# Optimization experiments

Measured on AMD Instinct MI355X. Metric: run time of the kernel, lower is better.

## Reference

```python
import jax, jax.numpy as jnp
import numpy as np

N, E, H, C, NG = 50000, 800000, 4, 64, 32
HC = H * C  # 256


def setup_inputs() -> dict:
    key = jax.random.key(0)
    ks = jax.random.split(key, 32)
    f32 = jnp.float32
    def rn(k, shape, s=0.1):
        return jax.random.normal(k, shape, dtype=f32) * s
    inp = {}
    inp['x'] = jax.random.normal(ks[0], (N, 4), dtype=f32)
    inp['edge_index'] = jax.random.randint(ks[1], (2, E), 0, N, dtype=jnp.int32)
    inp['edge_attr'] = jax.random.normal(ks[2], (E, 1), dtype=f32)
    inp['batch'] = jnp.sort(jax.random.randint(ks[3], (N,), 0, NG, dtype=jnp.int32))
    # encoder
    inp['enc_w'] = rn(ks[4], (4, 64)); inp['enc_b'] = rn(ks[5], (64,))
    # GATv2 layer 1: in 64 -> H*C (lin_l source, lin_r target, lin_edge, att, bias)
    inp['g1_wl'] = rn(ks[6], (64, HC)); inp['g1_bl'] = rn(ks[7], (HC,))
    inp['g1_wr'] = rn(ks[8], (64, HC)); inp['g1_br'] = rn(ks[9], (HC,))
    inp['g1_we'] = rn(ks[10], (1, HC))
    inp['g1_att'] = rn(ks[11], (H, C))
    inp['g1_bias'] = rn(ks[12], (HC,))
    # GATv2 layer 2: in 256 -> H*C
    inp['g2_wl'] = rn(ks[13], (HC, HC)); inp['g2_bl'] = rn(ks[14], (HC,))
    inp['g2_wr'] = rn(ks[15], (HC, HC)); inp['g2_br'] = rn(ks[16], (HC,))
    inp['g2_we'] = rn(ks[17], (1, HC))
    inp['g2_att'] = rn(ks[18], (H, C))
    inp['g2_bias'] = rn(ks[19], (HC,))
    # post MLP: 256 -> 128 (LayerNorm, ReLU) -> 64 (ReLU)
    inp['p1_w'] = rn(ks[20], (HC, 128)); inp['p1_b'] = rn(ks[21], (128,))
    inp['ln_g'] = jnp.ones((128,), dtype=f32); inp['ln_b'] = jnp.zeros((128,), dtype=f32)
    inp['p2_w'] = rn(ks[22], (128, 64)); inp['p2_b'] = rn(ks[23], (64,))
    return inp


def _gatv2_layer(x, src, dst, eattr, wl, bl, wr, br, we, att, bias):
    # PyG GATv2Conv: alpha_e = att . leaky_relu(lin_l(x_src) + lin_r(x_dst) + lin_edge(e))
    n = x.shape[0]
    xl = (x @ wl + bl).reshape(n, H, C)   # source-side messages
    xr = (x @ wr + br).reshape(n, H, C)   # target-side
    e = (eattr @ we).reshape(-1, H, C)
    m = jax.nn.leaky_relu(xl[src] + xr[dst] + e, 0.2)        # [E',H,C]
    alpha = jnp.einsum('ehc,hc->eh', m, att)                  # [E',H]
    amax = jax.lax.stop_gradient(jax.ops.segment_max(alpha, dst, num_segments=n))
    ex = jnp.exp(alpha - amax[dst])
    den = jax.ops.segment_sum(ex, dst, num_segments=n)
    a = ex / den[dst]                                          # softmax per dst node
    out = jax.ops.segment_sum(a[:, :, None] * xl[src], dst, num_segments=n)
    return out.reshape(n, HC) + bias


def reference(x, edge_index, edge_attr, batch, enc_w, enc_b,
              g1_wl, g1_bl, g1_wr, g1_br, g1_we, g1_att, g1_bias,
              g2_wl, g2_bl, g2_wr, g2_br, g2_we, g2_att, g2_bias,
              p1_w, p1_b, ln_g, ln_b, p2_w, p2_b):
    n = x.shape[0]
    src0, dst0 = edge_index[0], edge_index[1]
    # PyG default add_self_loops=True with fill_value='mean' for edge_attr
    deg = jnp.maximum(jax.ops.segment_sum(jnp.ones_like(edge_attr[:, 0]), dst0, num_segments=n), 1.0)
    loop_attr = jax.ops.segment_sum(edge_attr, dst0, num_segments=n) / deg[:, None]
    idx = jnp.arange(n, dtype=src0.dtype)
    src = jnp.concatenate([src0, idx]); dst = jnp.concatenate([dst0, idx])
    eattr = jnp.concatenate([edge_attr, loop_attr], axis=0)
    h = jax.nn.relu(x @ enc_w + enc_b)
    h = jax.nn.relu(_gatv2_layer(h, src, dst, eattr, g1_wl, g1_bl, g1_wr, g1_br, g1_we, g1_att, g1_bias))
    h = jax.nn.relu(_gatv2_layer(h, src, dst, eattr, g2_wl, g2_bl, g2_wr, g2_br, g2_we, g2_att, g2_bias))
    # global mean pool over graphs
    cnt = jnp.maximum(jax.ops.segment_sum(jnp.ones((n,), h.dtype), batch, num_segments=NG), 1.0)
    g = jax.ops.segment_sum(h, batch, num_segments=NG) / cnt[:, None]
    # post MLP (dropout is identity in eval)
    z = g @ p1_w + p1_b
    mu = jnp.mean(z, axis=-1, keepdims=True)
    var = jnp.mean((z - mu) ** 2, axis=-1, keepdims=True)
    z = (z - mu) / jnp.sqrt(var + 1e-5) * ln_g + ln_b
    z = jax.nn.relu(z)
    z = jax.nn.relu(z @ p2_w + p2_b)
    return z
```

## Files before the change

kernel.cpp:

```cpp
#include <hip/hip_runtime.h>

#define CDIV(a,b) (((a)+(b)-1)/(b))

typedef __bf16 bf16_t;
typedef bf16_t bf16x8 __attribute__((ext_vector_type(8)));
typedef bf16_t bf16x4 __attribute__((ext_vector_type(4)));
typedef float floatx4 __attribute__((ext_vector_type(4)));
typedef float floatx2 __attribute__((ext_vector_type(2)));

__device__ __forceinline__ int sigma(int p) {
    return ((p >> 7) << 7) + ((p & 7) << 4) + ((p >> 3) & 15);
}

__global__ void k_deg(const int* __restrict__ ei, const float* __restrict__ ea,
                      float* __restrict__ deg, float* __restrict__ lsum, int E) {
    int e = blockIdx.x * 256 + threadIdx.x;
    if (e >= E) return;
    int d = ei[E + e];
    atomicAdd(&deg[d], 1.0f);
    atomicAdd(&lsum[d], ea[e]);
}

__global__ void k_loopattr(float* __restrict__ lsum, const float* __restrict__ deg, int n) {
    int i = blockIdx.x * 256 + threadIdx.x;
    if (i >= n) return;
    lsum[i] = lsum[i] / fmaxf(deg[i], 1.0f);
}

__global__ void k_scanA(const float* __restrict__ deg, int* __restrict__ part, int n) {
    __shared__ int sh[256];
    int t = threadIdx.x;
    int i = blockIdx.x * 256 + t;
    int v = (i < n) ? (int)deg[i] + 1 : 0;
    sh[t] = v;
    __syncthreads();
    for (int d = 128; d > 0; d >>= 1) { if (t < d) sh[t] += sh[t + d]; __syncthreads(); }
    if (t == 0) part[blockIdx.x] = sh[0];
}
__global__ void k_scanB(int* __restrict__ part, int nb) {
    __shared__ int sh[256];
    int t = threadIdx.x;
    int v = (t < nb) ? part[t] : 0;
    sh[t] = v;
    __syncthreads();
    for (int d = 1; d < 256; d <<= 1) {
        int u = (t >= d) ? sh[t - d] : 0;
        __syncthreads();
        sh[t] += u;
        __syncthreads();
    }
    if (t < nb) part[t] = sh[t] - v;
}
__global__ void k_scanC(const float* __restrict__ deg, const int* __restrict__ part,
                        int* __restrict__ off, int n) {
    __shared__ int sh[256];
    int t = threadIdx.x;
    int i = blockIdx.x * 256 + t;
    int v = (i < n) ? (int)deg[i] + 1 : 0;
    sh[t] = v;
    __syncthreads();
    for (int d = 1; d < 256; d <<= 1) {
        int u = (t >= d) ? sh[t - d] : 0;
        __syncthreads();
        sh[t] += u;
        __syncthreads();
    }
    int excl = part[blockIdx.x] + sh[t] - v;
    if (i < n) off[i] = excl;
    if (i == n - 1) off[n] = excl + v;
}

__global__ void k_fill(const int* __restrict__ ei, const float* __restrict__ ea,
                       const float* __restrict__ lattr, const int* __restrict__ off,
                       int* __restrict__ cursor, int* __restrict__ csr_src,
                       float* __restrict__ csr_ea, int E, int n) {
    int e = blockIdx.x * 256 + threadIdx.x;
    int EE = E + n;
    if (e >= EE) return;
    int s, d; float a;
    if (e < E) { s = ei[e]; d = ei[E + e]; a = ea[e]; }
    else       { s = e - E; d = s;         a = lattr[s]; }
    int pos = off[d] + atomicAdd(&cursor[d], 1);
    csr_src[pos] = s;
    csr_ea[pos] = a;
}

__global__ void k_enc(const float* __restrict__ x, const float* __restrict__ w,
                      const float* __restrict__ b, bf16_t* __restrict__ h0, int n) {
    int idx = blockIdx.x * 256 + threadIdx.x;
    if (idx >= n * 64) return;
    int nn = idx >> 6, j = idx & 63;
    const float* xr = x + (size_t)nn * 4;
    float s = b[j];
#pragma unroll
    for (int k = 0; k < 4; ++k) s = fmaf(xr[k], w[k * 64 + j], s);
    h0[idx] = (bf16_t)fmaxf(s, 0.0f);
}

__global__ void k_wcast2(const float* __restrict__ Wl, const float* __restrict__ Wr,
                         const float* __restrict__ bl, const float* __restrict__ br,
                         bf16_t* __restrict__ Wt, float* __restrict__ bias2,
                         int K, int kshift, int permK,
                         const float* __restrict__ we, const float* __restrict__ att,
                         const float* __restrict__ cb,
                         float* __restrict__ wep, float* __restrict__ attp,
                         float* __restrict__ cbp) {
    int idx = blockIdx.x * 256 + threadIdx.x;
    if (idx < 512) bias2[idx] = (idx < 256) ? bl[idx] : br[idx - 256];
    if (idx < 256) {
        int sg = sigma(idx);
        wep[idx] = we[sg]; attp[idx] = att[sg]; cbp[idx] = cb[sg];
    }
    if (idx >= 512 * K) return;
    int nn = idx >> kshift, k = idx & (K - 1);
    int ks = permK ? sigma(k) : k;
    float v = (nn < 256) ? Wl[ks * 256 + nn] : Wr[ks * 256 + (nn - 256)];
    Wt[idx] = (bf16_t)v;
}

__global__ __launch_bounds__(256) void k_gemm_mfma(
        const bf16_t* __restrict__ Hb, const bf16_t* __restrict__ Wt,
        const float* __restrict__ bias2, bf16_t* __restrict__ XL,
        bf16_t* __restrict__ XR, int nrows, int K) {
    __shared__ bf16_t As[128 * 32];
    __shared__ bf16_t Bs[128 * 32];
    int tid = threadIdx.x;
    int w = tid >> 6, lane = tid & 63;
    int quad = lane >> 4, m = lane & 15;
    int row0 = blockIdx.x * 128;
    int n0 = blockIdx.y * 128;
    floatx4 acc[2][8];
#pragma unroll
    for (int rt = 0; rt < 2; ++rt)
#pragma unroll
        for (int ct = 0; ct < 8; ++ct)
            acc[rt][ct] = (floatx4){0.f, 0.f, 0.f, 0.f};

    for (int k0 = 0; k0 < K; k0 += 32) {
        __syncthreads();
#pragma unroll
        for (int i = 0; i < 2; ++i) {
            int c = tid + i * 256;
            int r = c >> 2, kc = c & 3;
            int sw = (kc + (r >> 1)) & 3;
            int gr = row0 + r; if (gr >= nrows) gr = nrows - 1;
            bf16x8 v = *(const bf16x8*)&Hb[(size_t)gr * K + k0 + kc * 8];
            *(bf16x8*)&As[r * 32 + sw * 8] = v;
        }
#pragma unroll
        for (int i = 0; i < 2; ++i) {
            int c = tid + i * 256;
            int r = c >> 2, kc = c & 3;
            int sw = (kc + (r >> 1)) & 3;
            bf16x8 v = *(const bf16x8*)&Wt[(size_t)(n0 + r) * K + k0 + kc * 8];
            *(bf16x8*)&Bs[r * 32 + sw * 8] = v;
        }
        __syncthreads();
        bf16x8 af[2], bfr[8];
#pragma unroll
        for (int rt = 0; rt < 2; ++rt) {
            int ar = w * 32 + rt * 16 + m;
            af[rt] = *(bf16x8*)&As[ar * 32 + (((quad + (ar >> 1)) & 3) * 8)];
        }
#pragma unroll
        for (int ct = 0; ct < 8; ++ct) {
            int br = ct * 16 + m;
            bfr[ct] = *(bf16x8*)&Bs[br * 32 + (((quad + (br >> 1)) & 3) * 8)];
        }
#pragma unroll
        for (int ct = 0; ct < 8; ++ct) {
            acc[0][ct] = __builtin_amdgcn_mfma_f32_16x16x32_bf16(af[0], bfr[ct], acc[0][ct], 0, 0, 0);
            acc[1][ct] = __builtin_amdgcn_mfma_f32_16x16x32_bf16(af[1], bfr[ct], acc[1][ct], 0, 0, 0);
        }
    }
    int tile = (n0 >> 7) & 1;
    bf16_t* dst = (n0 < 256) ? XL : XR;
    float bv[8];
#pragma unroll
    for (int ct = 0; ct < 8; ++ct) bv[ct] = bias2[n0 + ct * 16 + m];
#pragma unroll
    for (int rt = 0; rt < 2; ++rt) {
#pragma unroll
        for (int i = 0; i < 4; ++i) {
            int row = row0 + w * 32 + rt * 16 + quad * 4 + i;
            if (row < nrows) {
                bf16x8 v;
#pragma unroll
                for (int ct = 0; ct < 8; ++ct) v[ct] = (bf16_t)(acc[rt][ct][i] + bv[ct]);
                *(bf16x8*)&dst[(size_t)row * 256 + tile * 128 + m * 8] = v;
            }
        }
    }
}

__device__ __forceinline__ void edge_step(
        int p, const int* __restrict__ csr_src, const float* __restrict__ csr_ea,
        const bf16_t* __restrict__ XL, int lane8,
        floatx2 xr01, floatx2 xr23, floatx2 wv01, floatx2 wv23,
        floatx2 av01, floatx2 av23,
        float& s, floatx2& a01, floatx2& a23) {
    int src = csr_src[p];
    float eav = csr_ea[p];
    uint2 u = *(const uint2*)((const char*)XL + (size_t)src * 512 + lane8);
    floatx2 x01, x23;
    x01.x = __uint_as_float(u.x << 16);
    x01.y = __uint_as_float(u.x & 0xffff0000u);
    x23.x = __uint_as_float(u.y << 16);
    x23.y = __uint_as_float(u.y & 0xffff0000u);
    floatx2 t01 = x01 + xr01 + eav * wv01;
    floatx2 t23 = x23 + xr23 + eav * wv23;
    t01 = __builtin_elementwise_max(t01, 0.2f * t01);
    t23 = __builtin_elementwise_max(t23, 0.2f * t23);
    floatx2 d = t01 * av01 + t23 * av23;
    float al = d.x + d.y;
    al += __shfl_xor(al, 2);
    al += __shfl_xor(al, 4);
    al += __shfl_xor(al, 8);
    al += __shfl_xor(al, 16);
    float wg = exp2f(al);
    s += wg;
    a01 += wg * x01;
    a23 += wg * x23;
}

__global__ void k_conv(const bf16_t* __restrict__ XL, const bf16_t* __restrict__ XR,
                       const float* __restrict__ wep, const float* __restrict__ attp,
                       const int* __restrict__ csr_src, const float* __restrict__ csr_ea,
                       const int* __restrict__ off, const float* __restrict__ cbp,
                       bf16_t* __restrict__ outb, int n) {
    int wid = (blockIdx.x * 256 + threadIdx.x) >> 6;
    int lane = threadIdx.x & 63;
    if (wid >= n) return;
    int lane8 = lane * 8;
    uint2 ur = *(const uint2*)((const char*)XR + (size_t)wid * 512 + lane8);
    floatx2 xr01, xr23;
    xr01.x = __uint_as_float(ur.x << 16);
    xr01.y = __uint_as_float(ur.x & 0xffff0000u);
    xr23.x = __uint_as_float(ur.y << 16);
    xr23.y = __uint_as_float(ur.y & 0xffff0000u);
    float4 wv = ((const float4*)wep)[lane];
    float4 av = ((const float4*)attp)[lane];
    floatx2 wv01 = {wv.x, wv.y}, wv23 = {wv.z, wv.w};
    floatx2 av01 = {av.x * 1.44269504f, av.y * 1.44269504f};
    floatx2 av23 = {av.z * 1.44269504f, av.w * 1.44269504f};
    int p0 = off[wid], p1 = off[wid + 1];
    float s = 0.f;
    floatx2 a01 = {0.f, 0.f}, a23 = {0.f, 0.f};
    int p = p0;
    for (; p + 1 < p1; p += 2) {
        edge_step(p,     csr_src, csr_ea, XL, lane8, xr01, xr23, wv01, wv23, av01, av23, s, a01, a23);
        edge_step(p + 1, csr_src, csr_ea, XL, lane8, xr01, xr23, wv01, wv23, av01, av23, s, a01, a23);
    }
    if (p < p1)
        edge_step(p,     csr_src, csr_ea, XL, lane8, xr01, xr23, wv01, wv23, av01, av23, s, a01, a23);
    float inv = 1.0f / s;
    float4 bv = ((const float4*)cbp)[lane];
    float o0 = fmaxf(fmaf(a01.x, inv, bv.x), 0.f);
    float o1 = fmaxf(fmaf(a01.y, inv, bv.y), 0.f);
    float o2 = fmaxf(fmaf(a23.x, inv, bv.z), 0.f);
    float o3 = fmaxf(fmaf(a23.y, inv, bv.w), 0.f);
    bf16x4 ob;
    ob.x = (bf16_t)o0; ob.y = (bf16_t)o1; ob.z = (bf16_t)o2; ob.w = (bf16_t)o3;
    *(bf16x4*)&outb[(size_t)wid * 256 + lane * 4] = ob;
}

__global__ void k_pool(const bf16_t* __restrict__ h, const int* __restrict__ batch,
                       float* __restrict__ gsum, float* __restrict__ gcnt, int n) {
    int j = threadIdx.x;
    int start = blockIdx.x * 64;
    if (start >= n) return;
    int end = start + 64; if (end > n) end = n;
    int cur = batch[start];
    float acc = 0.0f, cnt = 0.0f;
    for (int i = start; i < end; ++i) {
        int g = batch[i];
        if (g != cur) {
            atomicAdd(&gsum[cur * 256 + j], acc);
            if (j == 0) atomicAdd(&gcnt[cur], cnt);
            acc = 0.0f; cnt = 0.0f; cur = g;
        }
        acc += (float)h[(size_t)i * 256 + j];
        cnt += 1.0f;
    }
    atomicAdd(&gsum[cur * 256 + j], acc);
    if (j == 0) atomicAdd(&gcnt[cur], cnt);
}

__global__ void k_mlp(const float* __restrict__ gsum, const float* __restrict__ gcnt,
                      const float* __restrict__ p1w, const float* __restrict__ p1b,
                      const float* __restrict__ lng, const float* __restrict__ lnb,
                      const float* __restrict__ p2w, const float* __restrict__ p2b,
                      float* __restrict__ out) {
    int g = blockIdx.x;
    int t = threadIdx.x;
    __shared__ float gv[256];
    __shared__ float z[128];
    __shared__ float red[128];
    float invc = 1.0f / fmaxf(gcnt[g], 1.0f);
    gv[sigma(t)]       = gsum[g * 256 + t] * invc;
    gv[sigma(t + 128)] = gsum[g * 256 + 128 + t] * invc;
    __syncthreads();
    float z1 = p1b[t];
    for (int k = 0; k < 256; ++k) z1 = fmaf(gv[k], p1w[k * 128 + t], z1);
    red[t] = z1;
    __syncthreads();
    for (int d = 64; d > 0; d >>= 1) { if (t < d) red[t] += red[t + d]; __syncthreads(); }
    float mu = red[0] * (1.0f / 128.0f);
    __syncthreads();
    float dz = z1 - mu;
    red[t] = dz * dz;
    __syncthreads();
    for (int d = 64; d > 0; d >>= 1) { if (t < d) red[t] += red[t + d]; __syncthreads(); }
    float var = red[0] * (1.0f / 128.0f);
    float zn = dz * rsqrtf(var + 1e-5f) * lng[t] + lnb[t];
    z[t] = fmaxf(zn, 0.0f);
    __syncthreads();
    if (t < 64) {
        float o = p2b[t];
        for (int k = 0; k < 128; ++k) o = fmaf(z[k], p2w[k * 64 + t], o);
        out[g * 64 + t] = fmaxf(o, 0.0f);
    }
}

extern "C" void kernel_launch(void* const* d_in, const int* in_sizes, int n_in,
                              void* d_out, int out_size, void* d_ws, size_t ws_size,
                              hipStream_t stream) {
    const float* x      = (const float*)d_in[0];
    const int*   ei     = (const int*)d_in[1];
    const float* ea     = (const float*)d_in[2];
    const int*   batch  = (const int*)d_in[3];
    const float* enc_w  = (const float*)d_in[4];
    const float* enc_b  = (const float*)d_in[5];
    const float* g1_wl  = (const float*)d_in[6];
    const float* g1_bl  = (const float*)d_in[7];
    const float* g1_wr  = (const float*)d_in[8];
    const float* g1_br  = (const float*)d_in[9];
    const float* g1_we  = (const float*)d_in[10];
    const float* g1_att = (const float*)d_in[11];
    const float* g1_bias= (const float*)d_in[12];
    const float* g2_wl  = (const float*)d_in[13];
    const float* g2_bl  = (const float*)d_in[14];
    const float* g2_wr  = (const float*)d_in[15];
    const float* g2_br  = (const float*)d_in[16];
    const float* g2_we  = (const float*)d_in[17];
    const float* g2_att = (const float*)d_in[18];
    const float* g2_bias= (const float*)d_in[19];
    const float* p1_w   = (const float*)d_in[20];
    const float* p1_b   = (const float*)d_in[21];
    const float* ln_g   = (const float*)d_in[22];
    const float* ln_b   = (const float*)d_in[23];
    const float* p2_w   = (const float*)d_in[24];
    const float* p2_b   = (const float*)d_in[25];
    float* out = (float*)d_out;

    const int N  = in_sizes[3];
    const int E  = in_sizes[1] / 2;
    const int EE = E + N;
    const int NB = CDIV(N, 256);

    bf16_t* XL  = (bf16_t*)d_ws;
    bf16_t* XR  = XL + (size_t)N * 256;
    bf16_t* Hb  = XR + (size_t)N * 256;
    bf16_t* Wt  = Hb + (size_t)N * 256;
    float* csr_ea= (float*)(Wt + 512 * 256);
    float* bias2 = csr_ea + EE;
    float* wep   = bias2 + 512;
    float* attp  = wep + 256;
    float* cbp   = attp + 256;
    float* deg   = cbp + 256;
    float* lsum  = deg + N;
    float* gsum  = lsum + N;
    float* gcnt  = gsum + 32 * 256;
    int*   cursor= (int*)(gcnt + 32);
    int*   part  = cursor + N;
    int*   off   = part + 256;
    int*   csr_src = off + (N + 1);

    hipMemsetAsync(deg, 0, (size_t)(3 * N + 32 * 256 + 32) * sizeof(float), stream);

    k_deg<<<CDIV(E, 256), 256, 0, stream>>>(ei, ea, deg, lsum, E);
    k_loopattr<<<CDIV(N, 256), 256, 0, stream>>>(lsum, deg, N);
    k_scanA<<<NB, 256, 0, stream>>>(deg, part, N);
    k_scanB<<<1, 256, 0, stream>>>(part, NB);
    k_scanC<<<NB, 256, 0, stream>>>(deg, part, off, N);
    k_fill<<<CDIV(EE, 256), 256, 0, stream>>>(ei, ea, lsum, off, cursor, csr_src, csr_ea, E, N);
    k_enc<<<CDIV(N * 64, 256), 256, 0, stream>>>(x, enc_w, enc_b, Hb, N);

    dim3 ggrid(CDIV(N, 128), 4);

    k_wcast2<<<CDIV(512 * 64, 256), 256, 0, stream>>>(g1_wl, g1_wr, g1_bl, g1_br, Wt, bias2,
                                                      64, 6, 0, g1_we, g1_att, g1_bias,
                                                      wep, attp, cbp);
    k_gemm_mfma<<<ggrid, 256, 0, stream>>>(Hb, Wt, bias2, XL, XR, N, 64);
    k_conv<<<CDIV(N, 4), 256, 0, stream>>>(XL, XR, wep, attp, csr_src, csr_ea, off, cbp, Hb, N);

    k_wcast2<<<CDIV(512 * 256, 256), 256, 0, stream>>>(g2_wl, g2_wr, g2_bl, g2_br, Wt, bias2,
                                                       256, 8, 1, g2_we, g2_att, g2_bias,
                                                       wep, attp, cbp);
    k_gemm_mfma<<<ggrid, 256, 0, stream>>>(Hb, Wt, bias2, XL, XR, N, 256);
    k_conv<<<CDIV(N, 4), 256, 0, stream>>>(XL, XR, wep, attp, csr_src, csr_ea, off, cbp, Hb, N);

    k_pool<<<CDIV(N, 64), 256, 0, stream>>>(Hb, batch, gsum, gcnt, N);
    k_mlp<<<32, 128, 0, stream>>>(gsum, gcnt, p1_w, p1_b, ln_g, ln_b, p2_w, p2_b, out);
}
```

Measured before the change: 510.9 us.

## Split conv wavefront into two half-waves processing alternate edges with 16-byte gathers

The aggregation kernel now has each 32-lane half of a wavefront handle a different edge, each lane owning 8 channels loaded as one 16-byte gather. This halves the shuffle reduction depth per edge and doubles the edges in flight. The GEMM output layout and channel permutation (sigma2) change to match, and the half-wave partial sums are combined with a cross-half shuffle at the end. Pooling blocks also shrink to 32 rows for more parallelism. The cost is odd-degree padding work and extra final shuffles.

```diff
diff --git a/kernel.cpp b/kernel.cpp
--- a/kernel.cpp
+++ b/kernel.cpp
@@ -8,8 +8,16 @@
 typedef float floatx4 __attribute__((ext_vector_type(4)));
 typedef float floatx2 __attribute__((ext_vector_type(2)));
 
-__device__ __forceinline__ int sigma(int p) {
-    return ((p >> 7) << 7) + ((p & 7) << 4) + ((p >> 3) & 15);
+__device__ __forceinline__ int sigma2(int p) {
+    int tile = p >> 7, hh = (p >> 6) & 1, m = (p >> 2) & 15, c = p & 3;
+    return tile * 128 + (hh * 4 + c) * 16 + m;
+}
+
+__device__ __forceinline__ floatx2 up2(unsigned v) {
+    floatx2 r;
+    r.x = __uint_as_float(v << 16);
+    r.y = __uint_as_float(v & 0xffff0000u);
+    return r;
 }
 
 __global__ void k_deg(const int* __restrict__ ei, const float* __restrict__ ea,
@@ -108,12 +116,12 @@
     int idx = blockIdx.x * 256 + threadIdx.x;
     if (idx < 512) bias2[idx] = (idx < 256) ? bl[idx] : br[idx - 256];
     if (idx < 256) {
-        int sg = sigma(idx);
+        int sg = sigma2(idx);
         wep[idx] = we[sg]; attp[idx] = att[sg]; cbp[idx] = cb[sg];
     }
     if (idx >= 512 * K) return;
     int nn = idx >> kshift, k = idx & (K - 1);
-    int ks = permK ? sigma(k) : k;
+    int ks = permK ? sigma2(k) : k;
     float v = (nn < 256) ? Wl[ks * 256 + nn] : Wr[ks * 256 + (nn - 256)];
     Wt[idx] = (bf16_t)v;
 }
@@ -184,43 +192,50 @@
         for (int i = 0; i < 4; ++i) {
             int row = row0 + w * 32 + rt * 16 + quad * 4 + i;
             if (row < nrows) {
-                bf16x8 v;
-#pragma unroll
-                for (int ct = 0; ct < 8; ++ct) v[ct] = (bf16_t)(acc[rt][ct][i] + bv[ct]);
-                *(bf16x8*)&dst[(size_t)row * 256 + tile * 128 + m * 8] = v;
+                bf16x4 v0, v1;
+#pragma unroll
+                for (int ct = 0; ct < 4; ++ct) {
+                    v0[ct] = (bf16_t)(acc[rt][ct][i] + bv[ct]);
+                    v1[ct] = (bf16_t)(acc[rt][ct + 4][i] + bv[ct + 4]);
+                }
+                *(bf16x4*)&dst[(size_t)row * 256 + tile * 128 + m * 4] = v0;
+                *(bf16x4*)&dst[(size_t)row * 256 + tile * 128 + 64 + m * 4] = v1;
             }
         }
     }
 }
 
-__device__ __forceinline__ void edge_step(
-        int p, const int* __restrict__ csr_src, const float* __restrict__ csr_ea,
-        const bf16_t* __restrict__ XL, int lane8,
-        floatx2 xr01, floatx2 xr23, floatx2 wv01, floatx2 wv23,
-        floatx2 av01, floatx2 av23,
-        float& s, floatx2& a01, floatx2& a23) {
-    int src = csr_src[p];
-    float eav = csr_ea[p];
-    uint2 u = *(const uint2*)((const char*)XL + (size_t)src * 512 + lane8);
-    floatx2 x01, x23;
-    x01.x = __uint_as_float(u.x << 16);
-    x01.y = __uint_as_float(u.x & 0xffff0000u);
-    x23.x = __uint_as_float(u.y << 16);
-    x23.y = __uint_as_float(u.y & 0xffff0000u);
+__device__ __forceinline__ void pair_step(
+        int p, int p1, int half, int loff,
+        const int* __restrict__ csr_src, const float* __restrict__ csr_ea,
+        const bf16_t* __restrict__ XL,
+        floatx2 xr01, floatx2 xr23, floatx2 xr45, floatx2 xr67,
+        floatx2 wv01, floatx2 wv23, floatx2 wv45, floatx2 wv67,
+        floatx2 av01, floatx2 av23, floatx2 av45, floatx2 av67,
+        float& s, floatx2& a01, floatx2& a23, floatx2& a45, floatx2& a67) {
+    int idx = p + half;
+    bool valid = idx < p1;
+    int idc = valid ? idx : p1 - 1;
+    int src = csr_src[idc];
+    float eav = csr_ea[idc];
+    uint4 u = *(const uint4*)((const char*)XL + (size_t)src * 512 + loff);
+    floatx2 x01 = up2(u.x), x23 = up2(u.y), x45 = up2(u.z), x67 = up2(u.w);
     floatx2 t01 = x01 + xr01 + eav * wv01;
     floatx2 t23 = x23 + xr23 + eav * wv23;
+    floatx2 t45 = x45 + xr45 + eav * wv45;
+    floatx2 t67 = x67 + xr67 + eav * wv67;
     t01 = __builtin_elementwise_max(t01, 0.2f * t01);
     t23 = __builtin_elementwise_max(t23, 0.2f * t23);
-    floatx2 d = t01 * av01 + t23 * av23;
+    t45 = __builtin_elementwise_max(t45, 0.2f * t45);
+    t67 = __builtin_elementwise_max(t67, 0.2f * t67);
+    floatx2 d = t01 * av01 + t23 * av23 + t45 * av45 + t67 * av67;
     float al = d.x + d.y;
+    al += __shfl_xor(al, 1);
     al += __shfl_xor(al, 2);
     al += __shfl_xor(al, 4);
-    al += __shfl_xor(al, 8);
-    al += __shfl_xor(al, 16);
-    float wg = exp2f(al);
+    float wg = valid ? exp2f(al) : 0.0f;
     s += wg;
-    a01 += wg * x01;
-    a23 += wg * x23;
+    a01 += wg * x01; a23 += wg * x23; a45 += wg * x45; a67 += wg * x67;
 }
 
 __global__ void k_conv(const bf16_t* __restrict__ XL, const bf16_t* __restrict__ XR,
@@ -231,45 +246,57 @@
     int wid = (blockIdx.x * 256 + threadIdx.x) >> 6;
     int lane = threadIdx.x & 63;
     if (wid >= n) return;
-    int lane8 = lane * 8;
-    uint2 ur = *(const uint2*)((const char*)XR + (size_t)wid * 512 + lane8);
-    floatx2 xr01, xr23;
-    xr01.x = __uint_as_float(ur.x << 16);
-    xr01.y = __uint_as_float(ur.x & 0xffff0000u);
-    xr23.x = __uint_as_float(ur.y << 16);
-    xr23.y = __uint_as_float(ur.y & 0xffff0000u);
-    float4 wv = ((const float4*)wep)[lane];
-    float4 av = ((const float4*)attp)[lane];
-    floatx2 wv01 = {wv.x, wv.y}, wv23 = {wv.z, wv.w};
-    floatx2 av01 = {av.x * 1.44269504f, av.y * 1.44269504f};
-    floatx2 av23 = {av.z * 1.44269504f, av.w * 1.44269504f};
+    int l = lane & 31, half = lane >> 5;
+    int loff = l * 16;
+    uint4 ur = *(const uint4*)((const char*)XR + (size_t)wid * 512 + loff);
+    floatx2 xr01 = up2(ur.x), xr23 = up2(ur.y), xr45 = up2(ur.z), xr67 = up2(ur.w);
+    float4 wa = ((const float4*)wep)[2 * l], wb = ((const float4*)wep)[2 * l + 1];
+    float4 aa = ((const float4*)attp)[2 * l], ab = ((const float4*)attp)[2 * l + 1];
+    floatx2 wv01 = {wa.x, wa.y}, wv23 = {wa.z, wa.w};
+    floatx2 wv45 = {wb.x, wb.y}, wv67 = {wb.z, wb.w};
+    const float LOG2E = 1.44269504f;
+    floatx2 av01 = {aa.x * LOG2E, aa.y * LOG2E}, av23 = {aa.z * LOG2E, aa.w * LOG2E};
+    floatx2 av45 = {ab.x * LOG2E, ab.y * LOG2E}, av67 = {ab.z * LOG2E, ab.w * LOG2E};
     int p0 = off[wid], p1 = off[wid + 1];
     float s = 0.f;
-    floatx2 a01 = {0.f, 0.f}, a23 = {0.f, 0.f};
+    floatx2 a01 = {0.f, 0.f}, a23 = {0.f, 0.f}, a45 = {0.f, 0.f}, a67 = {0.f, 0.f};
     int p = p0;
-    for (; p + 1 < p1; p += 2) {
-        edge_step(p,     csr_src, csr_ea, XL, lane8, xr01, xr23, wv01, wv23, av01, av23, s, a01, a23);
-        edge_step(p + 1, csr_src, csr_ea, XL, lane8, xr01, xr23, wv01, wv23, av01, av23, s, a01, a23);
-    }
-    if (p < p1)
-        edge_step(p,     csr_src, csr_ea, XL, lane8, xr01, xr23, wv01, wv23, av01, av23, s, a01, a23);
-    float inv = 1.0f / s;
-    float4 bv = ((const float4*)cbp)[lane];
-    float o0 = fmaxf(fmaf(a01.x, inv, bv.x), 0.f);
-    float o1 = fmaxf(fmaf(a01.y, inv, bv.y), 0.f);
-    float o2 = fmaxf(fmaf(a23.x, inv, bv.z), 0.f);
-    float o3 = fmaxf(fmaf(a23.y, inv, bv.w), 0.f);
-    bf16x4 ob;
-    ob.x = (bf16_t)o0; ob.y = (bf16_t)o1; ob.z = (bf16_t)o2; ob.w = (bf16_t)o3;
-    *(bf16x4*)&outb[(size_t)wid * 256 + lane * 4] = ob;
+    for (; p + 4 <= p1; p += 4) {
+        pair_step(p,     p1, half, loff, csr_src, csr_ea, XL, xr01, xr23, xr45, xr67,
+                  wv01, wv23, wv45, wv67, av01, av23, av45, av67, s, a01, a23, a45, a67);
+        pair_step(p + 2, p1, half, loff, csr_src, csr_ea, XL, xr01, xr23, xr45, xr67,
+                  wv01, wv23, wv45, wv67, av01, av23, av45, av67, s, a01, a23, a45, a67);
+    }
+    for (; p < p1; p += 2)
+        pair_step(p,     p1, half, loff, csr_src, csr_ea, XL, xr01, xr23, xr45, xr67,
+                  wv01, wv23, wv45, wv67, av01, av23, av45, av67, s, a01, a23, a45, a67);
+    s += __shfl_xor(s, 32);
+    a01.x += __shfl_xor(a01.x, 32); a01.y += __shfl_xor(a01.y, 32);
+    a23.x += __shfl_xor(a23.x, 32); a23.y += __shfl_xor(a23.y, 32);
+    a45.x += __shfl_xor(a45.x, 32); a45.y += __shfl_xor(a45.y, 32);
+    a67.x += __shfl_xor(a67.x, 32); a67.y += __shfl_xor(a67.y, 32);
+    if (half == 0) {
+        float inv = 1.0f / s;
+        float4 ba = ((const float4*)cbp)[2 * l], bb = ((const float4*)cbp)[2 * l + 1];
+        bf16x8 ob;
+        ob[0] = (bf16_t)fmaxf(fmaf(a01.x, inv, ba.x), 0.f);
+        ob[1] = (bf16_t)fmaxf(fmaf(a01.y, inv, ba.y), 0.f);
+        ob[2] = (bf16_t)fmaxf(fmaf(a23.x, inv, ba.z), 0.f);
+        ob[3] = (bf16_t)fmaxf(fmaf(a23.y, inv, ba.w), 0.f);
+        ob[4] = (bf16_t)fmaxf(fmaf(a45.x, inv, bb.x), 0.f);
+        ob[5] = (bf16_t)fmaxf(fmaf(a45.y, inv, bb.y), 0.f);
+        ob[6] = (bf16_t)fmaxf(fmaf(a67.x, inv, bb.z), 0.f);
+        ob[7] = (bf16_t)fmaxf(fmaf(a67.y, inv, bb.w), 0.f);
+        *(bf16x8*)&outb[(size_t)wid * 256 + l * 8] = ob;
+    }
 }
 
 __global__ void k_pool(const bf16_t* __restrict__ h, const int* __restrict__ batch,
                        float* __restrict__ gsum, float* __restrict__ gcnt, int n) {
     int j = threadIdx.x;
-    int start = blockIdx.x * 64;
+    int start = blockIdx.x * 32;
     if (start >= n) return;
-    int end = start + 64; if (end > n) end = n;
+    int end = start + 32; if (end > n) end = n;
     int cur = batch[start];
     float acc = 0.0f, cnt = 0.0f;
     for (int i = start; i < end; ++i) {
@@ -297,8 +324,8 @@
     __shared__ float z[128];
     __shared__ float red[128];
     float invc = 1.0f / fmaxf(gcnt[g], 1.0f);
-    gv[sigma(t)]       = gsum[g * 256 + t] * invc;
-    gv[sigma(t + 128)] = gsum[g * 256 + 128 + t] * invc;
+    gv[sigma2(t)]       = gsum[g * 256 + t] * invc;
+    gv[sigma2(t + 128)] = gsum[g * 256 + 128 + t] * invc;
     __syncthreads();
     float z1 = p1b[t];
     for (int k = 0; k < 256; ++k) z1 = fmaf(gv[k], p1w[k * 128 + t], z1);
@@ -400,6 +427,6 @@
     k_gemm_mfma<<<ggrid, 256, 0, stream>>>(Hb, Wt, bias2, XL, XR, N, 256);
     k_conv<<<CDIV(N, 4), 256, 0, stream>>>(XL, XR, wep, attp, csr_src, csr_ea, off, cbp, Hb, N);
 
-    k_pool<<<CDIV(N, 64), 256, 0, stream>>>(Hb, batch, gsum, gcnt, N);
+    k_pool<<<CDIV(N, 32), 256, 0, stream>>>(Hb, batch, gsum, gcnt, N);
     k_mlp<<<32, 128, 0, stream>>>(gsum, gcnt, p1_w, p1_b, ln_g, ln_b, p2_w, p2_b, out);
 }
```

After: 512.2 us. Within noise of the previous version (+0.3%).
